# Kernel optimization log

Hardware: AMD Instinct MI355X
Metric: run time of the kernel (lower is better)

## Reference

```python
import jax, jax.numpy as jnp
import numpy as np

B, S, E, H, D = 4, 2048, 512, 8, 64
NEG = 1e13  # module uses -1e13, not -inf


def setup_inputs() -> dict:
    key = jax.random.key(0)
    ks = jax.random.split(key, 10)
    x = jax.random.normal(ks[0], (B, S, E), dtype=jnp.float32)
    padding_pos = jax.random.randint(ks[1], (B, S), 0, 2, dtype=jnp.int64)
    std = 0.01
    # weights stored [in, out]; torch Linear init: normal(0, 0.01) weights, default bias
    Wq = jax.random.normal(ks[2], (E, H * D), dtype=jnp.float32) * std
    Wk = jax.random.normal(ks[3], (E, H * D), dtype=jnp.float32) * std
    Wv = jax.random.normal(ks[4], (E, H * D), dtype=jnp.float32) * std
    Wo = jax.random.normal(ks[5], (H * D, E), dtype=jnp.float32) * std
    bq = jax.random.uniform(ks[6], (H * D,), dtype=jnp.float32, minval=-1, maxval=1) / np.sqrt(E)
    bk = jax.random.uniform(ks[7], (H * D,), dtype=jnp.float32, minval=-1, maxval=1) / np.sqrt(E)
    bv = jax.random.uniform(ks[8], (H * D,), dtype=jnp.float32, minval=-1, maxval=1) / np.sqrt(E)
    bo = jax.random.uniform(ks[9], (E,), dtype=jnp.float32, minval=-1, maxval=1) / np.sqrt(H * D)
    return {"x": x, "padding_pos": padding_pos, "Wq": Wq, "bq": bq, "Wk": Wk,
            "bk": bk, "Wv": Wv, "bv": bv, "Wo": Wo, "bo": bo}


def reference(x, padding_pos, Wq, bq, Wk, bk, Wv, bv, Wo, bo):
    b = x.shape[0]
    q = (x @ Wq + bq).reshape(b, S, H, D).transpose(0, 2, 1, 3)  # [B,H,S,D]
    k = (x @ Wk + bk).reshape(b, S, H, D).transpose(0, 2, 1, 3)
    v = (x @ Wv + bv).reshape(b, S, H, D).transpose(0, 2, 1, 3)
    att = jnp.einsum('bhqd,bhkd->bhqk', q, k) / jnp.sqrt(jnp.float32(D))
    pad = (padding_pos == 1)  # [B,S]
    # mask key columns and query rows (module masks both via broadcast fills)
    mask = pad[:, None, None, :] | pad[:, None, :, None]  # [B,1,S,S]
    att = jnp.where(mask, -NEG, att)
    att = jax.nn.softmax(att, axis=-1)
    out = jnp.einsum('bhqk,bhkd->bhqd', att, v)
    out = out.transpose(0, 2, 1, 3).reshape(b, S, H * D)
    return out @ Wo + bo
```

## Files before the change

### kernel.cpp

```cpp
#include <hip/hip_runtime.h>
#include <hip/hip_bf16.h>
#include <math.h>

#define Bb 4
#define Ss 2048
#define Ee 512
#define Hh 8
#define Dd 64
#define HD 512
#define Mm (Bb*Ss)
#define RPB 1536
#define TPB 12
#define QTMAX 24

using bf16x8 = __attribute__((ext_vector_type(8))) short;
using f32x4  = __attribute__((ext_vector_type(4))) float;

typedef __attribute__((address_space(1))) const unsigned int gu32;
typedef __attribute__((address_space(3))) unsigned int lu32;
__device__ inline void glds16(const void* g, void* l) {
    __builtin_amdgcn_global_load_lds((gu32*)g, (lu32*)l, 16, 0, 0);
}

__device__ inline unsigned short f2bf(float f) {
    unsigned int u = __float_as_uint(f);
    unsigned int r = (u + 0x7fffu + ((u >> 16) & 1u)) >> 16;
    return (unsigned short)r;
}
__device__ inline float bf2f(unsigned short u) {
    return __uint_as_float((unsigned int)u << 16);
}
__device__ inline unsigned int cvtpk(float a, float b) {
    float2 t; t.x = a; t.y = b;
    union { __hip_bfloat162 h; unsigned int u; } z;
    z.h = __float22bfloat162_rn(t);
    return z.u;
}

__global__ __launch_bounds__(256) void prep(
    const int* __restrict__ pad,
    const float* __restrict__ Wq, const float* __restrict__ Wk,
    const float* __restrict__ Wv, const float* __restrict__ Wo,
    unsigned short* __restrict__ Wt,
    int* __restrict__ idx, int* __restrict__ rank, int* __restrict__ cnt)
{
    __shared__ float T[64][68];
    const int bi = blockIdx.x, tid = threadIdx.x;

    if (bi < 256) {
        const int w = bi >> 6;
        const float* W = (w == 0) ? Wq : (w == 1) ? Wk : (w == 2) ? Wv : Wo;
        const int tk0 = ((bi >> 3) & 7) * 64, tn0 = (bi & 7) * 64;
        #pragma unroll
        for (int l = 0; l < 4; ++l) {
            int fi = tid + l * 256;
            int r = fi >> 4, c4 = (fi & 15) * 4;
            *(float4*)&T[r][c4] = *(const float4*)(W + (size_t)(tk0 + r) * Ee + tn0 + c4);
        }
        __syncthreads();
        #pragma unroll
        for (int l = 0; l < 4; ++l) {
            int fi = tid + l * 256;
            int r2 = fi >> 4, c4 = (fi & 15) * 4;
            uint2 o;
            o.x = cvtpk(T[c4 + 0][r2], T[c4 + 1][r2]);
            o.y = cvtpk(T[c4 + 2][r2], T[c4 + 3][r2]);
            *(uint2*)(Wt + (size_t)w * 262144 + (size_t)(tn0 + r2) * Ee + tk0 + c4) = o;
        }
    } else {
        const int b = bi - 256;
        int* sc = (int*)&T[0][0];
        int loc[8], c = 0;
        #pragma unroll
        for (int j = 0; j < 8; ++j) {
            loc[j] = pad[b * Ss + tid * 8 + j];
            c += (loc[j] == 0);
        }
        sc[tid] = c;
        __syncthreads();
        for (int s = 1; s < 256; s <<= 1) {
            int v = (tid >= s) ? sc[tid - s] : 0;
            __syncthreads();
            sc[tid] += v;
            __syncthreads();
        }
        int off = sc[tid] - c;
        #pragma unroll
        for (int j = 0; j < 8; ++j)
            if (loc[j] == 0) {
                idx[b * Ss + off] = tid * 8 + j;
                rank[b * Ss + tid * 8 + j] = off;
                ++off;
            }
        if (tid == 255) cnt[b] = sc[255];
    }
}

__global__ __launch_bounds__(256) void gatherx(
    const float* __restrict__ x, const int* __restrict__ pad,
    const int* __restrict__ rank,
    unsigned short* __restrict__ xc, float* __restrict__ xpart)
{
    const int bx = blockIdx.x, tid = threadIdx.x;
    const int b = bx >> 4, i = bx & 15;
    const int c8 = (tid & 63) * 8, grp = tid >> 6;
    __shared__ float sm[4][512];

    float a8[8] = {};
    for (int it = 0; it < 32; ++it) {
        int s = i * 128 + grp * 32 + it;
        const float* pr = x + ((size_t)b * Ss + s) * Ee + c8;
        float4 f0 = *(const float4*)pr;
        float4 f1 = *(const float4*)(pr + 4);
        a8[0] += f0.x; a8[1] += f0.y; a8[2] += f0.z; a8[3] += f0.w;
        a8[4] += f1.x; a8[5] += f1.y; a8[6] += f1.z; a8[7] += f1.w;
        if (pad[b * Ss + s] == 0) {
            int rk = rank[b * Ss + s];
            uint4 v;
            v.x = cvtpk(f0.x, f0.y); v.y = cvtpk(f0.z, f0.w);
            v.z = cvtpk(f1.x, f1.y); v.w = cvtpk(f1.z, f1.w);
            *(uint4*)(xc + ((size_t)b * RPB + rk) * Ee + c8) = v;
        }
    }
    #pragma unroll
    for (int j = 0; j < 8; ++j) sm[grp][c8 + j] = a8[j];
    __syncthreads();
    int c0 = tid * 2;
    float s0 = sm[0][c0] + sm[1][c0] + sm[2][c0] + sm[3][c0];
    float s1 = sm[0][c0 + 1] + sm[1][c0 + 1] + sm[2][c0 + 1] + sm[3][c0 + 1];
    float2 o; o.x = s0; o.y = s1;
    *(float2*)(xpart + (size_t)(b * 16 + i) * Ee + c0) = o;
}

__global__ __launch_bounds__(256) void gemm_qkvt(
    const unsigned short* __restrict__ xc, const unsigned short* __restrict__ Wt,
    const float* __restrict__ bq, const float* __restrict__ bk, const float* __restrict__ bv,
    const int* __restrict__ cnt, const float* __restrict__ xpart,
    unsigned short* __restrict__ qo, unsigned short* __restrict__ ko,
    unsigned short* __restrict__ vt, float* __restrict__ vmw)
{
    const int z = blockIdx.z;
    const int bx = blockIdx.x, by = blockIdx.y;
    const int b = bx / TPB, t12 = bx - b * TPB;
    const int cntb = cnt[b];
    const int tid = threadIdx.x, lane = tid & 63, wv = tid >> 6;
    const int quad = lane >> 4, l15 = lane & 15;
    const int wm = (wv >> 1) * 64, wn = (wv & 1) * 64;

    __shared__ unsigned short As0[128][32], Bs0[128][32];
    __shared__ unsigned short As1[128][32], Bs1[128][32];

    if (z == 2 && t12 == TPB - 1) {
        __shared__ float xm[512];
        for (int kk = tid; kk < 512; kk += 256) {
            float s = 0.f;
            #pragma unroll
            for (int p = 0; p < 16; ++p) s += xpart[(size_t)(b * 16 + p) * Ee + kk];
            xm[kk] = s;
        }
        __syncthreads();
        int c = by * 128 + (tid >> 1);
        int kh = (tid & 1) * 256;
        const unsigned short* wrow = Wt + (size_t)2 * 262144 + (size_t)c * Ee + kh;
        float s = 0.f;
        for (int kk = 0; kk < 256; ++kk) s += xm[kh + kk] * bf2f(wrow[kk]);
        s += __shfl_xor(s, 1);
        if (!(tid & 1)) vmw[(size_t)b * HD + c] = s * (1.0f / 2048.0f) + bv[c];
        return;
    }

    if (t12 * 128 >= cntb) return;

    const unsigned short *Ap, *Bp;
    if (z < 2) {
        Ap = xc + ((size_t)b * RPB + t12 * 128) * Ee;
        Bp = Wt + (size_t)z * 262144 + (size_t)by * 128 * Ee;
    } else {
        Ap = Wt + (size_t)2 * 262144 + (size_t)by * 128 * Ee;
        Bp = xc + ((size_t)b * RPB + t12 * 128) * Ee;
    }

    f32x4 acc[4][4] = {};

    auto stage = [&](unsigned short (&A)[128][32], unsigned short (&B)[128][32], int k0) {
        #pragma unroll
        for (int l = 0; l < 2; ++l) {
            int ci = tid + l * 256;
            int r = ci >> 2, ch = (ci & 3) * 8;
            glds16(Ap + (size_t)r * Ee + k0 + ch, &A[r][ch]);
            glds16(Bp + (size_t)r * Ee + k0 + ch, &B[r][ch]);
        }
    };
    auto compute = [&](const unsigned short (&A)[128][32], const unsigned short (&B)[128][32]) {
        bf16x8 af[4], bfr[4];
        #pragma unroll
        for (int ms = 0; ms < 4; ++ms) af[ms] = *(const bf16x8*)&A[wm + ms * 16 + l15][quad * 8];
        #pragma unroll
        for (int ns = 0; ns < 4; ++ns) bfr[ns] = *(const bf16x8*)&B[wn + ns * 16 + l15][quad * 8];
        #pragma unroll
        for (int ms = 0; ms < 4; ++ms)
            #pragma unroll
            for (int ns = 0; ns < 4; ++ns)
                acc[ms][ns] = __builtin_amdgcn_mfma_f32_16x16x32_bf16(af[ms], bfr[ns], acc[ms][ns], 0, 0, 0);
    };

    stage(As0, Bs0, 0);
    for (int ki = 0; ki < 16; ki += 2) {
        __syncthreads();
        if (ki + 1 < 16) stage(As1, Bs1, (ki + 1) * 32);
        compute(As0, Bs0);
        __syncthreads();
        if (ki + 2 < 16) stage(As0, Bs0, (ki + 2) * 32);
        compute(As1, Bs1);
    }

    if (z < 2) {
        const float* bias = z ? bk : bq;
        unsigned short* dst = z ? ko : qo;
        #pragma unroll
        for (int ns = 0; ns < 4; ++ns) {
            int col = by * 128 + wn + ns * 16 + l15;
            float bb = bias[col];
            #pragma unroll
            for (int ms = 0; ms < 4; ++ms) {
                #pragma unroll
                for (int r = 0; r < 4; ++r) {
                    int m = t12 * 128 + wm + ms * 16 + quad * 4 + r;
                    float val = acc[ms][ns][r] + bb;
                    if (z == 0) val *= 0.18033688f;
                    dst[((size_t)b * RPB + m) * HD + col] = f2bf(val);
                }
            }
        }
    } else {
        #pragma unroll
        for (int ms = 0; ms < 4; ++ms) {
            #pragma unroll
            for (int r = 0; r < 4; ++r) {
                int dg = by * 128 + wm + ms * 16 + quad * 4 + r;
                float bb = bv[dg];
                #pragma unroll
                for (int ns = 0; ns < 4; ++ns) {
                    int col = t12 * 128 + wn + ns * 16 + l15;
                    vt[((size_t)b * HD + dg) * RPB + col] = f2bf(acc[ms][ns][r] + bb);
                }
            }
        }
    }
}

__global__ __launch_bounds__(256) void attn(
    const unsigned short* __restrict__ qc, const unsigned short* __restrict__ kc,
    const unsigned short* __restrict__ vtc, const int* __restrict__ cnt,
    unsigned short* __restrict__ pO, float* __restrict__ pL)
{
    __shared__ unsigned short Ks[2][64][32], Vs[2][64][32];
    __shared__ float Ps[4][16][68];

    const int tid = threadIdx.x, wv = tid >> 6, lane = tid & 63;
    const int quad = lane >> 4, l15 = lane & 15;
    const int bh = blockIdx.x, b = bh >> 3, h = bh & 7;
    const int qt = blockIdx.y, half = blockIdx.z;
    const int cntb = cnt[b];
    if (qt * 64 >= cntb) return;

    const int tot = (cntb + 63) >> 6;
    const int hsplit = (tot + 1) >> 1;
    const int kstart = half ? hsplit : 0;
    const int kend = half ? tot : hsplit;

    const unsigned short* qrow = qc + ((size_t)b * RPB + qt * 64 + wv * 16 + l15) * HD + h * Dd;
    bf16x8 aq0 = *(const bf16x8*)(qrow + quad * 8);
    bf16x8 aq1 = *(const bf16x8*)(qrow + 32 + quad * 8);

    const unsigned short* kcb = kc + (size_t)b * RPB * HD + h * Dd;
    const unsigned short* vtb = vtc + ((size_t)b * HD + h * Dd) * RPB;

    float li[4] = {};
    f32x4 oacc[4] = {};

    for (int kt = kstart; kt < kend; ++kt) {
        const int k0 = kt * 64;
        __syncthreads();
        #pragma unroll
        for (int l = 0; l < 2; ++l) {
            int ci = tid + l * 256;
            int s = ci >> 8, row = (ci >> 2) & 63, ch = (ci & 3) * 8;
            glds16(kcb + (size_t)(k0 + row) * HD + s * 32 + ch, &Ks[s][row][ch]);
            glds16(vtb + (size_t)row * RPB + k0 + s * 32 + ch, &Vs[s][row][ch]);
        }
        __syncthreads();

        f32x4 sa[4];
        #pragma unroll
        for (int nt = 0; nt < 4; ++nt) {
            bf16x8 k0f = *(const bf16x8*)&Ks[0][nt * 16 + l15][quad * 8];
            bf16x8 k1f = *(const bf16x8*)&Ks[1][nt * 16 + l15][quad * 8];
            f32x4 zz = {0.f, 0.f, 0.f, 0.f};
            zz = __builtin_amdgcn_mfma_f32_16x16x32_bf16(aq0, k0f, zz, 0, 0, 0);
            zz = __builtin_amdgcn_mfma_f32_16x16x32_bf16(aq1, k1f, zz, 0, 0, 0);
            sa[nt] = zz;
        }

        if (kt == tot - 1 && (cntb & 63)) {
            #pragma unroll
            for (int nt = 0; nt < 4; ++nt) {
                bool bad = (k0 + nt * 16 + l15) >= cntb;
                #pragma unroll
                for (int r = 0; r < 4; ++r)
                    if (bad) sa[nt][r] = -1e30f;
            }
        }

        #pragma unroll
        for (int nt = 0; nt < 4; ++nt)
            #pragma unroll
            for (int r = 0; r < 4; ++r) {
                float p = exp2f(sa[nt][r]);
                sa[nt][r] = p;
                li[r] += p;
            }

        #pragma unroll
        for (int r = 0; r < 4; ++r) {
            int qr = quad * 4 + r;
            #pragma unroll
            for (int nt = 0; nt < 4; ++nt)
                Ps[wv][qr][nt * 16 + l15] = sa[nt][r];
        }
        float4 p0 = *(const float4*)&Ps[wv][l15][quad * 8];
        float4 p1 = *(const float4*)&Ps[wv][l15][quad * 8 + 4];
        float4 p2 = *(const float4*)&Ps[wv][l15][32 + quad * 8];
        float4 p3 = *(const float4*)&Ps[wv][l15][32 + quad * 8 + 4];
        union U8 { unsigned int u[4]; bf16x8 v8; };
        U8 ap0, ap1;
        ap0.u[0] = cvtpk(p0.x, p0.y); ap0.u[1] = cvtpk(p0.z, p0.w);
        ap0.u[2] = cvtpk(p1.x, p1.y); ap0.u[3] = cvtpk(p1.z, p1.w);
        ap1.u[0] = cvtpk(p2.x, p2.y); ap1.u[1] = cvtpk(p2.z, p2.w);
        ap1.u[2] = cvtpk(p3.x, p3.y); ap1.u[3] = cvtpk(p3.z, p3.w);

        #pragma unroll
        for (int nt = 0; nt < 4; ++nt) {
            bf16x8 v0f = *(const bf16x8*)&Vs[0][nt * 16 + l15][quad * 8];
            bf16x8 v1f = *(const bf16x8*)&Vs[1][nt * 16 + l15][quad * 8];
            oacc[nt] = __builtin_amdgcn_mfma_f32_16x16x32_bf16(ap0.v8, v0f, oacc[nt], 0, 0, 0);
            oacc[nt] = __builtin_amdgcn_mfma_f32_16x16x32_bf16(ap1.v8, v1f, oacc[nt], 0, 0, 0);
        }
    }

    const size_t pbase = (((size_t)bh * QTMAX + qt) * 2 + half) * 4096;
    const size_t lbase = (((size_t)bh * QTMAX + qt) * 2 + half) * 64;
    #pragma unroll
    for (int r = 0; r < 4; ++r) {
        float ls = li[r];
        ls += __shfl_xor(ls, 1);
        ls += __shfl_xor(ls, 2);
        ls += __shfl_xor(ls, 4);
        ls += __shfl_xor(ls, 8);
        int prow = wv * 16 + quad * 4 + r;
        if (l15 == 0) pL[lbase + prow] = ls;
        #pragma unroll
        for (int nt = 0; nt < 4; ++nt)
            pO[pbase + (size_t)prow * 64 + nt * 16 + l15] = f2bf(oacc[nt][r]);
    }
}

__global__ __launch_bounds__(256) void combine(
    const unsigned short* __restrict__ pO, const float* __restrict__ pL,
    const int* __restrict__ cnt, const float* __restrict__ vmw,
    const unsigned short* __restrict__ Wt, const float* __restrict__ bo,
    unsigned short* __restrict__ aoc, float* __restrict__ out_pad)
{
    const int bh = blockIdx.x, b = bh >> 3, h = bh & 7;
    const int y = blockIdx.y, tid = threadIdx.x;
    const int cntb = cnt[b];
    __shared__ float vm[512];

    if (y >= QTMAX) {
        if (h != 0) return;
        for (int t = tid; t < 512; t += 256) vm[t] = vmw[(size_t)b * HD + t];
        __syncthreads();
        int cc = (y - QTMAX) * 256 + tid;
        const unsigned short* wrow = Wt + (size_t)3 * 262144 + (size_t)cc * HD;
        float s = 0.f;
        #pragma unroll 8
        for (int k = 0; k < 512; ++k) s += vm[k] * bf2f(wrow[k]);
        out_pad[(size_t)b * Ee + cc] = s + bo[cc];
        return;
    }

    const int qt = y;
    if (qt * 64 >= cntb) return;
    const int row = tid >> 2, dch = (tid & 3) * 16;
    const int jq = qt * 64 + row;
    if (jq >= cntb) return;
    const size_t lb = ((size_t)bh * QTMAX + qt) * 2 * 64;
    float lsum = pL[lb + row] + pL[lb + 64 + row];
    float inv = (lsum > 0.f) ? 1.0f / lsum : 0.f;
    const size_t pb = ((size_t)bh * QTMAX + qt) * 2 * 4096 + (size_t)row * 64 + dch;
    union { uint4 q; unsigned short u[8]; } a0, a1, b0, b1;
    a0.q = *(const uint4*)(pO + pb);
    a1.q = *(const uint4*)(pO + pb + 8);
    b0.q = *(const uint4*)(pO + pb + 4096);
    b1.q = *(const uint4*)(pO + pb + 4096 + 8);
    uint4 o0, o1;
    float v0, v1;
    v0 = (bf2f(a0.u[0]) + bf2f(b0.u[0])) * inv; v1 = (bf2f(a0.u[1]) + bf2f(b0.u[1])) * inv;
    o0.x = cvtpk(v0, v1);
    v0 = (bf2f(a0.u[2]) + bf2f(b0.u[2])) * inv; v1 = (bf2f(a0.u[3]) + bf2f(b0.u[3])) * inv;
    o0.y = cvtpk(v0, v1);
    v0 = (bf2f(a0.u[4]) + bf2f(b0.u[4])) * inv; v1 = (bf2f(a0.u[5]) + bf2f(b0.u[5])) * inv;
    o0.z = cvtpk(v0, v1);
    v0 = (bf2f(a0.u[6]) + bf2f(b0.u[6])) * inv; v1 = (bf2f(a0.u[7]) + bf2f(b0.u[7])) * inv;
    o0.w = cvtpk(v0, v1);
    v0 = (bf2f(a1.u[0]) + bf2f(b1.u[0])) * inv; v1 = (bf2f(a1.u[1]) + bf2f(b1.u[1])) * inv;
    o1.x = cvtpk(v0, v1);
    v0 = (bf2f(a1.u[2]) + bf2f(b1.u[2])) * inv; v1 = (bf2f(a1.u[3]) + bf2f(b1.u[3])) * inv;
    o1.y = cvtpk(v0, v1);
    v0 = (bf2f(a1.u[4]) + bf2f(b1.u[4])) * inv; v1 = (bf2f(a1.u[5]) + bf2f(b1.u[5])) * inv;
    o1.z = cvtpk(v0, v1);
    v0 = (bf2f(a1.u[6]) + bf2f(b1.u[6])) * inv; v1 = (bf2f(a1.u[7]) + bf2f(b1.u[7])) * inv;
    o1.w = cvtpk(v0, v1);
    unsigned short* dst = aoc + ((size_t)b * RPB + jq) * HD + h * Dd + dch;
    *(uint4*)dst = o0;
    *(uint4*)(dst + 8) = o1;
}

__global__ __launch_bounds__(256) void gemm_out(
    const unsigned short* __restrict__ a_in, const unsigned short* __restrict__ Wt,
    const float* __restrict__ bo, const int* __restrict__ idx,
    const int* __restrict__ cnt, const int* __restrict__ pad,
    const float* __restrict__ out_pad, float* __restrict__ out)
{
    const int bx = blockIdx.x, by = blockIdx.y;
    const int tid = threadIdx.x;

    if (bx >= Bb * TPB) {
        if (by != 0) return;
        const int fb = bx - Bb * TPB;
        const int b = fb >> 3, seg = fb & 7;
        const int c0 = tid * 2;
        float2 op = *(const float2*)(out_pad + (size_t)b * Ee + c0);
        for (int r = 0; r < 256; ++r) {
            int s = seg * 256 + r;
            if (pad[b * Ss + s])
                *(float2*)(out + ((size_t)b * Ss + s) * Ee + c0) = op;
        }
        return;
    }

    const int b = bx / TPB, t12 = bx - b * TPB;
    const int cntb = cnt[b];
    if (t12 * 128 >= cntb) return;

    const unsigned short* Wz = Wt + (size_t)3 * 262144;
    const int m0 = t12 * 128, n0 = by * 128;
    const int lane = tid & 63, wv = tid >> 6;
    const int quad = lane >> 4, l15 = lane & 15;
    const int wm = (wv >> 1) * 64, wn = (wv & 1) * 64;
    const unsigned short* Ab = a_in + (size_t)b * RPB * HD;

    __shared__ unsigned short As0[128][32], Bs0[128][32];
    __shared__ unsigned short As1[128][32], Bs1[128][32];

    f32x4 acc[4][4] = {};

    auto stage = [&](unsigned short (&A)[128][32], unsigned short (&B)[128][32], int k0) {
        #pragma unroll
        for (int l = 0; l < 2; ++l) {
            int ci = tid + l * 256;
            int r = ci >> 2, ch = (ci & 3) * 8;
            glds16(Ab + (size_t)(m0 + r) * HD + k0 + ch, &A[r][ch]);
            glds16(Wz + (size_t)(n0 + r) * HD + k0 + ch, &B[r][ch]);
        }
    };
    auto compute = [&](const unsigned short (&A)[128][32], const unsigned short (&B)[128][32]) {
        bf16x8 af[4], bfr[4];
        #pragma unroll
        for (int ms = 0; ms < 4; ++ms) af[ms] = *(const bf16x8*)&A[wm + ms * 16 + l15][quad * 8];
        #pragma unroll
        for (int ns = 0; ns < 4; ++ns) bfr[ns] = *(const bf16x8*)&B[wn + ns * 16 + l15][quad * 8];
        #pragma unroll
        for (int ms = 0; ms < 4; ++ms)
            #pragma unroll
            for (int ns = 0; ns < 4; ++ns)
                acc[ms][ns] = __builtin_amdgcn_mfma_f32_16x16x32_bf16(af[ms], bfr[ns], acc[ms][ns], 0, 0, 0);
    };

    stage(As0, Bs0, 0);
    for (int ki = 0; ki < 16; ki += 2) {
        __syncthreads();
        if (ki + 1 < 16) stage(As1, Bs1, (ki + 1) * 32);
        compute(As0, Bs0);
        __syncthreads();
        if (ki + 2 < 16) stage(As0, Bs0, (ki + 2) * 32);
        compute(As1, Bs1);
    }

    #pragma unroll
    for (int ns = 0; ns < 4; ++ns) {
        int col = n0 + wn + ns * 16 + l15;
        float bb = bo[col];
        #pragma unroll
        for (int ms = 0; ms < 4; ++ms) {
            #pragma unroll
            for (int r = 0; r < 4; ++r) {
                int m = m0 + wm + ms * 16 + quad * 4 + r;
                if (m < cntb) {
                    int srow = idx[b * Ss + m];
                    out[((size_t)b * Ss + srow) * Ee + col] = acc[ms][ns][r] + bb;
                }
            }
        }
    }
}

extern "C" void kernel_launch(void* const* d_in, const int* in_sizes, int n_in,
                              void* d_out, int out_size, void* d_ws, size_t ws_size,
                              hipStream_t stream) {
    const float* x   = (const float*)d_in[0];
    const int*   pad = (const int*)  d_in[1];
    const float* Wq  = (const float*)d_in[2];
    const float* bq  = (const float*)d_in[3];
    const float* Wk  = (const float*)d_in[4];
    const float* bk  = (const float*)d_in[5];
    const float* Wv  = (const float*)d_in[6];
    const float* bv  = (const float*)d_in[7];
    const float* Wo  = (const float*)d_in[8];
    const float* bo  = (const float*)d_in[9];
    float* out = (float*)d_out;

    const size_t csz = (size_t)Bb * RPB * HD;
    unsigned short* Wt  = (unsigned short*)d_ws;
    unsigned short* qc  = Wt + 1048576;
    unsigned short* kc  = qc + csz;
    unsigned short* vtc = kc + csz;
    unsigned short* aoc = vtc + csz;
    unsigned short* xc  = aoc + csz;
    unsigned short* pO  = xc;
    unsigned short* tail = xc + 6291456;
    float* xpart = (float*)tail;
    int*   idxw  = (int*)(xpart + 64 * 512);
    int*   rankw = idxw + Mm;
    int*   cntw  = rankw + Mm;
    float* vmw   = (float*)(cntw + 4);
    float* opad  = vmw + Bb * HD;
    float* pLw   = opad + Bb * Ee;

    prep<<<260, 256, 0, stream>>>(pad, Wq, Wk, Wv, Wo, Wt, idxw, rankw, cntw);

    gatherx<<<64, 256, 0, stream>>>(x, pad, rankw, xc, xpart);

    dim3 g1(Bb * TPB, 4, 3);
    gemm_qkvt<<<g1, 256, 0, stream>>>(xc, Wt, bq, bk, bv, cntw, xpart, qc, kc, vtc, vmw);

    dim3 g2(Bb * Hh, QTMAX, 2);
    attn<<<g2, 256, 0, stream>>>(qc, kc, vtc, cntw, pO, pLw);

    dim3 g3(Bb * Hh, QTMAX + 2);
    combine<<<g3, 256, 0, stream>>>(pO, pLw, cntw, vmw, Wt, bo, aoc, opad);

    dim3 g4(Bb * TPB + 32, 4);
    gemm_out<<<g4, 256, 0, stream>>>(aoc, Wt, bo, idxw, cntw, pad, opad, out);
}
```

Before: 182.3 us.

## Shrink GEMM tiles to 64x64 and fuse split-KV combine into attention

The QKV and output projection GEMMs move from 128x128 to 64x64 tiles on a flattened 1D grid, which gives many more blocks to spread across the CUs. The separate combine kernel is removed. The second of the two attention halves for each query tile to finish now performs the normalisation and merge, detected with an atomic counter and a threadfence, and the padded-row output projection is folded into extra attention blocks. This saves one kernel launch and improves occupancy, at the cost of less data reuse per GEMM tile plus added atomics and fence overhead.

```diff
diff --git a/kernel.cpp b/kernel.cpp
--- a/kernel.cpp
+++ b/kernel.cpp
@@ -10,8 +10,9 @@
 #define HD 512
 #define Mm (Bb*Ss)
 #define RPB 1536
-#define TPB 12
 #define QTMAX 24
+#define AT 24
+#define NT 8
 
 using bf16x8 = __attribute__((ext_vector_type(8))) short;
 using f32x4  = __attribute__((ext_vector_type(4))) float;
@@ -42,7 +43,8 @@
     const float* __restrict__ Wq, const float* __restrict__ Wk,
     const float* __restrict__ Wv, const float* __restrict__ Wo,
     unsigned short* __restrict__ Wt,
-    int* __restrict__ idx, int* __restrict__ rank, int* __restrict__ cnt)
+    int* __restrict__ idx, int* __restrict__ rank, int* __restrict__ cnt,
+    int* __restrict__ pCnt)
 {
     __shared__ float T[64][68];
     const int bi = blockIdx.x, tid = threadIdx.x;
@@ -69,6 +71,7 @@
         }
     } else {
         const int b = bi - 256;
+        if (tid < 192) pCnt[b * 192 + tid] = 0;
         int* sc = (int*)&T[0][0];
         int loc[8], c = 0;
         #pragma unroll
@@ -140,17 +143,19 @@
     unsigned short* __restrict__ vt, float* __restrict__ vmw)
 {
     const int z = blockIdx.z;
-    const int bx = blockIdx.x, by = blockIdx.y;
-    const int b = bx / TPB, t12 = bx - b * TPB;
+    const int bx = blockIdx.x;
+    const int b = bx / 192, t = bx - b * 192;
+    const int at = (z < 2) ? (t >> 3) : (t & 7);
+    const int bt = (z < 2) ? (t & 7) : (t >> 3);
     const int cntb = cnt[b];
     const int tid = threadIdx.x, lane = tid & 63, wv = tid >> 6;
     const int quad = lane >> 4, l15 = lane & 15;
-    const int wm = (wv >> 1) * 64, wn = (wv & 1) * 64;
-
-    __shared__ unsigned short As0[128][32], Bs0[128][32];
-    __shared__ unsigned short As1[128][32], Bs1[128][32];
-
-    if (z == 2 && t12 == TPB - 1) {
+    const int wm = (wv >> 1) * 32, wn = (wv & 1) * 32;
+
+    __shared__ unsigned short As0[64][32], Bs0[64][32];
+    __shared__ unsigned short As1[64][32], Bs1[64][32];
+
+    if (z == 2 && bt == AT - 1) {
         __shared__ float xm[512];
         for (int kk = tid; kk < 512; kk += 256) {
             float s = 0.f;
@@ -159,48 +164,47 @@
             xm[kk] = s;
         }
         __syncthreads();
-        int c = by * 128 + (tid >> 1);
-        int kh = (tid & 1) * 256;
-        const unsigned short* wrow = Wt + (size_t)2 * 262144 + (size_t)c * Ee + kh;
+        int col = at * 64 + (tid >> 2);
+        int kh = (tid & 3) * 128;
+        const unsigned short* wrow = Wt + (size_t)2 * 262144 + (size_t)col * Ee + kh;
         float s = 0.f;
-        for (int kk = 0; kk < 256; ++kk) s += xm[kh + kk] * bf2f(wrow[kk]);
+        #pragma unroll 8
+        for (int kk = 0; kk < 128; ++kk) s += xm[kh + kk] * bf2f(wrow[kk]);
         s += __shfl_xor(s, 1);
-        if (!(tid & 1)) vmw[(size_t)b * HD + c] = s * (1.0f / 2048.0f) + bv[c];
+        s += __shfl_xor(s, 2);
+        if ((tid & 3) == 0) vmw[(size_t)b * HD + col] = s * (1.0f / 2048.0f) + bv[col];
         return;
     }
 
-    if (t12 * 128 >= cntb) return;
+    const int xcTile = (z < 2) ? at : bt;
+    if (xcTile * 64 >= cntb) return;
 
     const unsigned short *Ap, *Bp;
     if (z < 2) {
-        Ap = xc + ((size_t)b * RPB + t12 * 128) * Ee;
-        Bp = Wt + (size_t)z * 262144 + (size_t)by * 128 * Ee;
+        Ap = xc + ((size_t)b * RPB + at * 64) * Ee;
+        Bp = Wt + (size_t)z * 262144 + (size_t)bt * 64 * Ee;
     } else {
-        Ap = Wt + (size_t)2 * 262144 + (size_t)by * 128 * Ee;
-        Bp = xc + ((size_t)b * RPB + t12 * 128) * Ee;
-    }
-
-    f32x4 acc[4][4] = {};
-
-    auto stage = [&](unsigned short (&A)[128][32], unsigned short (&B)[128][32], int k0) {
-        #pragma unroll
-        for (int l = 0; l < 2; ++l) {
-            int ci = tid + l * 256;
-            int r = ci >> 2, ch = (ci & 3) * 8;
-            glds16(Ap + (size_t)r * Ee + k0 + ch, &A[r][ch]);
-            glds16(Bp + (size_t)r * Ee + k0 + ch, &B[r][ch]);
-        }
+        Ap = Wt + (size_t)2 * 262144 + (size_t)at * 64 * Ee;
+        Bp = xc + ((size_t)b * RPB + bt * 64) * Ee;
+    }
+
+    f32x4 acc[2][2] = {};
+
+    auto stage = [&](unsigned short (&A)[64][32], unsigned short (&B)[64][32], int k0) {
+        int r = tid >> 2, ch = (tid & 3) * 8;
+        glds16(Ap + (size_t)r * Ee + k0 + ch, &A[r][ch]);
+        glds16(Bp + (size_t)r * Ee + k0 + ch, &B[r][ch]);
     };
-    auto compute = [&](const unsigned short (&A)[128][32], const unsigned short (&B)[128][32]) {
-        bf16x8 af[4], bfr[4];
-        #pragma unroll
-        for (int ms = 0; ms < 4; ++ms) af[ms] = *(const bf16x8*)&A[wm + ms * 16 + l15][quad * 8];
-        #pragma unroll
-        for (int ns = 0; ns < 4; ++ns) bfr[ns] = *(const bf16x8*)&B[wn + ns * 16 + l15][quad * 8];
-        #pragma unroll
-        for (int ms = 0; ms < 4; ++ms)
-            #pragma unroll
-            for (int ns = 0; ns < 4; ++ns)
+    auto compute = [&](const unsigned short (&A)[64][32], const unsigned short (&B)[64][32]) {
+        bf16x8 af[2], bfr[2];
+        #pragma unroll
+        for (int ms = 0; ms < 2; ++ms) af[ms] = *(const bf16x8*)&A[wm + ms * 16 + l15][quad * 8];
+        #pragma unroll
+        for (int ns = 0; ns < 2; ++ns) bfr[ns] = *(const bf16x8*)&B[wn + ns * 16 + l15][quad * 8];
+        #pragma unroll
+        for (int ms = 0; ms < 2; ++ms)
+            #pragma unroll
+            for (int ns = 0; ns < 2; ++ns)
                 acc[ms][ns] = __builtin_amdgcn_mfma_f32_16x16x32_bf16(af[ms], bfr[ns], acc[ms][ns], 0, 0, 0);
     };
 
@@ -218,14 +222,14 @@
         const float* bias = z ? bk : bq;
         unsigned short* dst = z ? ko : qo;
         #pragma unroll
-        for (int ns = 0; ns < 4; ++ns) {
-            int col = by * 128 + wn + ns * 16 + l15;
+        for (int ns = 0; ns < 2; ++ns) {
+            int col = bt * 64 + wn + ns * 16 + l15;
             float bb = bias[col];
             #pragma unroll
-            for (int ms = 0; ms < 4; ++ms) {
+            for (int ms = 0; ms < 2; ++ms) {
                 #pragma unroll
                 for (int r = 0; r < 4; ++r) {
-                    int m = t12 * 128 + wm + ms * 16 + quad * 4 + r;
+                    int m = at * 64 + wm + ms * 16 + quad * 4 + r;
                     float val = acc[ms][ns][r] + bb;
                     if (z == 0) val *= 0.18033688f;
                     dst[((size_t)b * RPB + m) * HD + col] = f2bf(val);
@@ -234,14 +238,14 @@
         }
     } else {
         #pragma unroll
-        for (int ms = 0; ms < 4; ++ms) {
+        for (int ms = 0; ms < 2; ++ms) {
             #pragma unroll
             for (int r = 0; r < 4; ++r) {
-                int dg = by * 128 + wm + ms * 16 + quad * 4 + r;
+                int dg = at * 64 + wm + ms * 16 + quad * 4 + r;
                 float bb = bv[dg];
                 #pragma unroll
-                for (int ns = 0; ns < 4; ++ns) {
-                    int col = t12 * 128 + wn + ns * 16 + l15;
+                for (int ns = 0; ns < 2; ++ns) {
+                    int col = bt * 64 + wn + ns * 16 + l15;
                     vt[((size_t)b * HD + dg) * RPB + col] = f2bf(acc[ms][ns][r] + bb);
                 }
             }
@@ -252,15 +256,35 @@
 __global__ __launch_bounds__(256) void attn(
     const unsigned short* __restrict__ qc, const unsigned short* __restrict__ kc,
     const unsigned short* __restrict__ vtc, const int* __restrict__ cnt,
-    unsigned short* __restrict__ pO, float* __restrict__ pL)
+    unsigned short* __restrict__ pO, float* __restrict__ pL,
+    int* __restrict__ pCnt, const float* __restrict__ vmw,
+    const unsigned short* __restrict__ Wt, const float* __restrict__ bo,
+    float* __restrict__ opad, unsigned short* __restrict__ aoc)
 {
     __shared__ unsigned short Ks[2][64][32], Vs[2][64][32];
     __shared__ float Ps[4][16][68];
+    __shared__ int sOld;
 
     const int tid = threadIdx.x, wv = tid >> 6, lane = tid & 63;
     const int quad = lane >> 4, l15 = lane & 15;
     const int bh = blockIdx.x, b = bh >> 3, h = bh & 7;
     const int qt = blockIdx.y, half = blockIdx.z;
+
+    if (qt >= QTMAX) {
+        if (half || bh >= 8) return;
+        const int b2 = bh >> 1, seg = bh & 1;
+        float* vm = &Ps[0][0][0];
+        for (int t = tid; t < 512; t += 256) vm[t] = vmw[(size_t)b2 * HD + t];
+        __syncthreads();
+        int cc = seg * 256 + tid;
+        const unsigned short* wrow = Wt + (size_t)3 * 262144 + (size_t)cc * HD;
+        float s = 0.f;
+        #pragma unroll 8
+        for (int k = 0; k < 512; ++k) s += vm[k] * bf2f(wrow[k]);
+        opad[(size_t)b2 * Ee + cc] = s + bo[cc];
+        return;
+    }
+
     const int cntb = cnt[b];
     if (qt * 64 >= cntb) return;
 
@@ -363,67 +387,48 @@
         for (int nt = 0; nt < 4; ++nt)
             pO[pbase + (size_t)prow * 64 + nt * 16 + l15] = f2bf(oacc[nt][r]);
     }
-}
-
-__global__ __launch_bounds__(256) void combine(
-    const unsigned short* __restrict__ pO, const float* __restrict__ pL,
-    const int* __restrict__ cnt, const float* __restrict__ vmw,
-    const unsigned short* __restrict__ Wt, const float* __restrict__ bo,
-    unsigned short* __restrict__ aoc, float* __restrict__ out_pad)
-{
-    const int bh = blockIdx.x, b = bh >> 3, h = bh & 7;
-    const int y = blockIdx.y, tid = threadIdx.x;
-    const int cntb = cnt[b];
-    __shared__ float vm[512];
-
-    if (y >= QTMAX) {
-        if (h != 0) return;
-        for (int t = tid; t < 512; t += 256) vm[t] = vmw[(size_t)b * HD + t];
-        __syncthreads();
-        int cc = (y - QTMAX) * 256 + tid;
-        const unsigned short* wrow = Wt + (size_t)3 * 262144 + (size_t)cc * HD;
-        float s = 0.f;
-        #pragma unroll 8
-        for (int k = 0; k < 512; ++k) s += vm[k] * bf2f(wrow[k]);
-        out_pad[(size_t)b * Ee + cc] = s + bo[cc];
-        return;
-    }
-
-    const int qt = y;
-    if (qt * 64 >= cntb) return;
-    const int row = tid >> 2, dch = (tid & 3) * 16;
-    const int jq = qt * 64 + row;
-    if (jq >= cntb) return;
-    const size_t lb = ((size_t)bh * QTMAX + qt) * 2 * 64;
-    float lsum = pL[lb + row] + pL[lb + 64 + row];
-    float inv = (lsum > 0.f) ? 1.0f / lsum : 0.f;
-    const size_t pb = ((size_t)bh * QTMAX + qt) * 2 * 4096 + (size_t)row * 64 + dch;
-    union { uint4 q; unsigned short u[8]; } a0, a1, b0, b1;
-    a0.q = *(const uint4*)(pO + pb);
-    a1.q = *(const uint4*)(pO + pb + 8);
-    b0.q = *(const uint4*)(pO + pb + 4096);
-    b1.q = *(const uint4*)(pO + pb + 4096 + 8);
-    uint4 o0, o1;
-    float v0, v1;
-    v0 = (bf2f(a0.u[0]) + bf2f(b0.u[0])) * inv; v1 = (bf2f(a0.u[1]) + bf2f(b0.u[1])) * inv;
-    o0.x = cvtpk(v0, v1);
-    v0 = (bf2f(a0.u[2]) + bf2f(b0.u[2])) * inv; v1 = (bf2f(a0.u[3]) + bf2f(b0.u[3])) * inv;
-    o0.y = cvtpk(v0, v1);
-    v0 = (bf2f(a0.u[4]) + bf2f(b0.u[4])) * inv; v1 = (bf2f(a0.u[5]) + bf2f(b0.u[5])) * inv;
-    o0.z = cvtpk(v0, v1);
-    v0 = (bf2f(a0.u[6]) + bf2f(b0.u[6])) * inv; v1 = (bf2f(a0.u[7]) + bf2f(b0.u[7])) * inv;
-    o0.w = cvtpk(v0, v1);
-    v0 = (bf2f(a1.u[0]) + bf2f(b1.u[0])) * inv; v1 = (bf2f(a1.u[1]) + bf2f(b1.u[1])) * inv;
-    o1.x = cvtpk(v0, v1);
-    v0 = (bf2f(a1.u[2]) + bf2f(b1.u[2])) * inv; v1 = (bf2f(a1.u[3]) + bf2f(b1.u[3])) * inv;
-    o1.y = cvtpk(v0, v1);
-    v0 = (bf2f(a1.u[4]) + bf2f(b1.u[4])) * inv; v1 = (bf2f(a1.u[5]) + bf2f(b1.u[5])) * inv;
-    o1.z = cvtpk(v0, v1);
-    v0 = (bf2f(a1.u[6]) + bf2f(b1.u[6])) * inv; v1 = (bf2f(a1.u[7]) + bf2f(b1.u[7])) * inv;
-    o1.w = cvtpk(v0, v1);
-    unsigned short* dst = aoc + ((size_t)b * RPB + jq) * HD + h * Dd + dch;
-    *(uint4*)dst = o0;
-    *(uint4*)(dst + 8) = o1;
+
+    __threadfence();
+    __syncthreads();
+    if (tid == 0) sOld = atomicAdd(&pCnt[bh * QTMAX + qt], 1);
+    __syncthreads();
+    if (sOld == 1) {
+        __threadfence();
+        const int row = tid >> 2, dch = (tid & 3) * 16;
+        const int jq = qt * 64 + row;
+        if (jq < cntb) {
+            const size_t lb = ((size_t)bh * QTMAX + qt) * 2 * 64;
+            float lsum = pL[lb + row] + pL[lb + 64 + row];
+            float inv = (lsum > 0.f) ? 1.0f / lsum : 0.f;
+            const size_t pb = ((size_t)bh * QTMAX + qt) * 2 * 4096 + (size_t)row * 64 + dch;
+            union { uint4 q; unsigned short u[8]; } a0, a1, b0, b1;
+            a0.q = *(const uint4*)(pO + pb);
+            a1.q = *(const uint4*)(pO + pb + 8);
+            b0.q = *(const uint4*)(pO + pb + 4096);
+            b1.q = *(const uint4*)(pO + pb + 4096 + 8);
+            uint4 o0, o1;
+            float v0, v1;
+            v0 = (bf2f(a0.u[0]) + bf2f(b0.u[0])) * inv; v1 = (bf2f(a0.u[1]) + bf2f(b0.u[1])) * inv;
+            o0.x = cvtpk(v0, v1);
+            v0 = (bf2f(a0.u[2]) + bf2f(b0.u[2])) * inv; v1 = (bf2f(a0.u[3]) + bf2f(b0.u[3])) * inv;
+            o0.y = cvtpk(v0, v1);
+            v0 = (bf2f(a0.u[4]) + bf2f(b0.u[4])) * inv; v1 = (bf2f(a0.u[5]) + bf2f(b0.u[5])) * inv;
+            o0.z = cvtpk(v0, v1);
+            v0 = (bf2f(a0.u[6]) + bf2f(b0.u[6])) * inv; v1 = (bf2f(a0.u[7]) + bf2f(b0.u[7])) * inv;
+            o0.w = cvtpk(v0, v1);
+            v0 = (bf2f(a1.u[0]) + bf2f(b1.u[0])) * inv; v1 = (bf2f(a1.u[1]) + bf2f(b1.u[1])) * inv;
+            o1.x = cvtpk(v0, v1);
+            v0 = (bf2f(a1.u[2]) + bf2f(b1.u[2])) * inv; v1 = (bf2f(a1.u[3]) + bf2f(b1.u[3])) * inv;
+            o1.y = cvtpk(v0, v1);
+            v0 = (bf2f(a1.u[4]) + bf2f(b1.u[4])) * inv; v1 = (bf2f(a1.u[5]) + bf2f(b1.u[5])) * inv;
+            o1.z = cvtpk(v0, v1);
+            v0 = (bf2f(a1.u[6]) + bf2f(b1.u[6])) * inv; v1 = (bf2f(a1.u[7]) + bf2f(b1.u[7])) * inv;
+            o1.w = cvtpk(v0, v1);
+            unsigned short* dst = aoc + ((size_t)b * RPB + jq) * HD + h * Dd + dch;
+            *(uint4*)dst = o0;
+            *(uint4*)(dst + 8) = o1;
+        }
+    }
 }
 
 __global__ __launch_bounds__(256) void gemm_out(
@@ -432,12 +437,11 @@
     const int* __restrict__ cnt, const int* __restrict__ pad,
     const float* __restrict__ out_pad, float* __restrict__ out)
 {
-    const int bx = blockIdx.x, by = blockIdx.y;
+    const int bx = blockIdx.x;
     const int tid = threadIdx.x;
 
-    if (bx >= Bb * TPB) {
-        if (by != 0) return;
-        const int fb = bx - Bb * TPB;
+    if (bx >= Bb * 192) {
+        const int fb = bx - Bb * 192;
         const int b = fb >> 3, seg = fb & 7;
         const int c0 = tid * 2;
         float2 op = *(const float2*)(out_pad + (size_t)b * Ee + c0);
@@ -449,41 +453,38 @@
         return;
     }
 
-    const int b = bx / TPB, t12 = bx - b * TPB;
+    const int b = bx / 192, t = bx - b * 192;
+    const int at = t >> 3, bt = t & 7;
     const int cntb = cnt[b];
-    if (t12 * 128 >= cntb) return;
+    if (at * 64 >= cntb) return;
 
     const unsigned short* Wz = Wt + (size_t)3 * 262144;
-    const int m0 = t12 * 128, n0 = by * 128;
     const int lane = tid & 63, wv = tid >> 6;
     const int quad = lane >> 4, l15 = lane & 15;
-    const int wm = (wv >> 1) * 64, wn = (wv & 1) * 64;
-    const unsigned short* Ab = a_in + (size_t)b * RPB * HD;
-
-    __shared__ unsigned short As0[128][32], Bs0[128][32];
-    __shared__ unsigned short As1[128][32], Bs1[128][32];
-
-    f32x4 acc[4][4] = {};
-
-    auto stage = [&](unsigned short (&A)[128][32], unsigned short (&B)[128][32], int k0) {
-        #pragma unroll
-        for (int l = 0; l < 2; ++l) {
-            int ci = tid + l * 256;
-            int r = ci >> 2, ch = (ci & 3) * 8;
-            glds16(Ab + (size_t)(m0 + r) * HD + k0 + ch, &A[r][ch]);
-            glds16(Wz + (size_t)(n0 + r) * HD + k0 + ch, &B[r][ch]);
-        }
+    const int wm = (wv >> 1) * 32, wn = (wv & 1) * 32;
+    const unsigned short* Ab = a_in + ((size_t)b * RPB + at * 64) * HD;
+    const unsigned short* Bp = Wz + (size_t)bt * 64 * HD;
+
+    __shared__ unsigned short As0[64][32], Bs0[64][32];
+    __shared__ unsigned short As1[64][32], Bs1[64][32];
+
+    f32x4 acc[2][2] = {};
+
+    auto stage = [&](unsigned short (&A)[64][32], unsigned short (&B)[64][32], int k0) {
+        int r = tid >> 2, ch = (tid & 3) * 8;
+        glds16(Ab + (size_t)r * HD + k0 + ch, &A[r][ch]);
+        glds16(Bp + (size_t)r * HD + k0 + ch, &B[r][ch]);
     };
-    auto compute = [&](const unsigned short (&A)[128][32], const unsigned short (&B)[128][32]) {
-        bf16x8 af[4], bfr[4];
-        #pragma unroll
-        for (int ms = 0; ms < 4; ++ms) af[ms] = *(const bf16x8*)&A[wm + ms * 16 + l15][quad * 8];
-        #pragma unroll
-        for (int ns = 0; ns < 4; ++ns) bfr[ns] = *(const bf16x8*)&B[wn + ns * 16 + l15][quad * 8];
-        #pragma unroll
-        for (int ms = 0; ms < 4; ++ms)
-            #pragma unroll
-            for (int ns = 0; ns < 4; ++ns)
+    auto compute = [&](const unsigned short (&A)[64][32], const unsigned short (&B)[64][32]) {
+        bf16x8 af[2], bfr[2];
+        #pragma unroll
+        for (int ms = 0; ms < 2; ++ms) af[ms] = *(const bf16x8*)&A[wm + ms * 16 + l15][quad * 8];
+        #pragma unroll
+        for (int ns = 0; ns < 2; ++ns) bfr[ns] = *(const bf16x8*)&B[wn + ns * 16 + l15][quad * 8];
+        #pragma unroll
+        for (int ms = 0; ms < 2; ++ms)
+            #pragma unroll
+            for (int ns = 0; ns < 2; ++ns)
                 acc[ms][ns] = __builtin_amdgcn_mfma_f32_16x16x32_bf16(af[ms], bfr[ns], acc[ms][ns], 0, 0, 0);
     };
 
@@ -498,14 +499,14 @@
     }
 
     #pragma unroll
-    for (int ns = 0; ns < 4; ++ns) {
-        int col = n0 + wn + ns * 16 + l15;
+    for (int ns = 0; ns < 2; ++ns) {
+        int col = bt * 64 + wn + ns * 16 + l15;
         float bb = bo[col];
         #pragma unroll
-        for (int ms = 0; ms < 4; ++ms) {
+        for (int ms = 0; ms < 2; ++ms) {
             #pragma unroll
             for (int r = 0; r < 4; ++r) {
-                int m = m0 + wm + ms * 16 + quad * 4 + r;
+                int m = at * 64 + wm + ms * 16 + quad * 4 + r;
                 if (m < cntb) {
                     int srow = idx[b * Ss + m];
                     out[((size_t)b * Ss + srow) * Ee + col] = acc[ms][ns][r] + bb;
@@ -546,20 +547,18 @@
     float* vmw   = (float*)(cntw + 4);
     float* opad  = vmw + Bb * HD;
     float* pLw   = opad + Bb * Ee;
-
-    prep<<<260, 256, 0, stream>>>(pad, Wq, Wk, Wv, Wo, Wt, idxw, rankw, cntw);
+    int*   pCnt  = (int*)(pLw + 32 * QTMAX * 2 * 64);
+
+    prep<<<260, 256, 0, stream>>>(pad, Wq, Wk, Wv, Wo, Wt, idxw, rankw, cntw, pCnt);
 
     gatherx<<<64, 256, 0, stream>>>(x, pad, rankw, xc, xpart);
 
-    dim3 g1(Bb * TPB, 4, 3);
+    dim3 g1(Bb * 192, 1, 3);
     gemm_qkvt<<<g1, 256, 0, stream>>>(xc, Wt, bq, bk, bv, cntw, xpart, qc, kc, vtc, vmw);
 
-    dim3 g2(Bb * Hh, QTMAX, 2);
-    attn<<<g2, 256, 0, stream>>>(qc, kc, vtc, cntw, pO, pLw);
-
-    dim3 g3(Bb * Hh, QTMAX + 2);
-    combine<<<g3, 256, 0, stream>>>(pO, pLw, cntw, vmw, Wt, bo, aoc, opad);
-
-    dim3 g4(Bb * TPB + 32, 4);
-    gemm_out<<<g4, 256, 0, stream>>>(aoc, Wt, bo, idxw, cntw, pad, opad, out);
-}
+    dim3 g2(Bb * Hh, QTMAX + 1, 2);
+    attn<<<g2, 256, 0, stream>>>(qc, kc, vtc, cntw, pO, pLw, pCnt, vmw, Wt, bo, opad, aoc);
+
+    dim3 g3(Bb * 192 + 32, 1);
+    gemm_out<<<g3, 256, 0, stream>>>(aoc, Wt, bo, idxw, cntw, pad, opad, out);
+}
```

Result: slower. 368.7 us (+102.2%).
